# Performance work log

Hardware: AMD Instinct MI355X
Metric: run time of the kernel (lower is better)

## Reference

```python
import jax, jax.numpy as jnp
import numpy as np

N = 4096      # num_nodes (tokens)
D = 1024      # in_features
GC1 = 1024    # gc hidden sizes
GC2 = 1024
FC1 = 512     # fc hidden
NUM_CLASSES = 2
FW = 8        # forward band width
BW = 8        # backward band width


def setup_inputs() -> dict:
    key = jax.random.key(0)
    ks = jax.random.split(key, 6)
    s = 0.02
    return {
        "x": jax.random.normal(ks[0], (N, D), jnp.float32),
        # sequential band weights, initialized to 0.5 as in the module
        "fw_w": 0.5 * jnp.ones((FW,), jnp.float32),
        "bw_w": 0.5 * jnp.ones((BW,), jnp.float32),
        # graph-conv layer weights (linear: h @ W + b, then A @ .)
        "gc_w1": s * jax.random.normal(ks[1], (D, GC1), jnp.float32),
        "gc_b1": jnp.zeros((GC1,), jnp.float32),
        "gc_w2": s * jax.random.normal(ks[2], (GC1, GC2), jnp.float32),
        "gc_b2": jnp.zeros((GC2,), jnp.float32),
        # fully-connected head
        "fc_w1": s * jax.random.normal(ks[3], (GC2, FC1), jnp.float32),
        "fc_b1": jnp.zeros((FC1,), jnp.float32),
        "fc_w2": s * jax.random.normal(ks[4], (FC1, NUM_CLASSES), jnp.float32),
        "fc_b2": jnp.zeros((NUM_CLASSES,), jnp.float32),
    }


def build_adjacency(fw_w, bw_w, n):
    # banded adjacency: self-loops + forward superdiagonals + backward subdiagonals,
    # then symmetric normalization D^{-1/2} A D^{-1/2}
    a = jnp.eye(n, dtype=fw_w.dtype)
    for j in range(fw_w.shape[0]):          # small fixed band loop (FW)
        a = a + fw_w[j] * jnp.eye(n, k=j + 1, dtype=fw_w.dtype)
    for j in range(bw_w.shape[0]):          # small fixed band loop (BW)
        a = a + bw_w[j] * jnp.eye(n, k=-(j + 1), dtype=bw_w.dtype)
    d = a.sum(axis=1) ** -0.5               # row degrees
    return d[:, None] * a * d[None, :]


def reference(x, fw_w, bw_w, gc_w1, gc_b1, gc_w2, gc_b2, fc_w1, fc_b1, fc_w2, fc_b2):
    a = build_adjacency(fw_w, bw_w, x.shape[0])          # [N, N]
    # GC layers: selu(A @ (H W + b)); dropout=0.0 -> identity
    h = jax.nn.selu(a @ (x @ gc_w1 + gc_b1))             # [N, GC1]
    h = jax.nn.selu(a @ (h @ gc_w2 + gc_b2))             # [N, GC2]
    pooled = h.mean(axis=0)                              # mean pooling over nodes
    z = jax.nn.selu(pooled @ fc_w1 + fc_b1)              # [FC1]
    return z @ fc_w2 + fc_b2                             # [NUM_CLASSES] logits
```

## Files before the change

kernel.cpp:

```cpp
#include <hip/hip_runtime.h>
#include <stdint.h>

#define NND 4096
#define DIM 1024
#define FC1N 512

typedef __attribute__((ext_vector_type(8))) short short8;
typedef __attribute__((ext_vector_type(4))) float floatx4;
typedef unsigned short u16;
typedef unsigned int u32;

__device__ __forceinline__ u16 f2bf(float f) {
    union { float f; u32 u; } a; a.f = f;
    u32 u = a.u;
    return (u16)((u + 0x7fffu + ((u >> 16) & 1u)) >> 16);
}
__device__ __forceinline__ float bf2f(u16 h) {
    union { u32 u; float f; } a; a.u = ((u32)h) << 16; return a.f;
}
__device__ __forceinline__ float selu_f(float x) {
    const float lam = 1.0507009873554805f;
    const float alp = 1.6732632423543772f;
    return x > 0.f ? lam * x : lam * alp * (expf(x) - 1.f);
}
__device__ __forceinline__ void async16(const u16* g, u16* l) {
    __builtin_amdgcn_global_load_lds((const __attribute__((address_space(1))) u32*)g,
                                     (__attribute__((address_space(3))) u32*)l, 16, 0, 0);
}

__global__ void k_prep(const float* __restrict__ x, const float* __restrict__ w1,
                       const float* __restrict__ w2, u16* __restrict__ Xb,
                       u16* __restrict__ W1t, u16* __restrict__ W2t,
                       float* __restrict__ zero_base) {
    int b = blockIdx.x, t = threadIdx.x;
    if (b < 512) {
        const float4* xin = (const float4*)x;
        ushort4* xo = (ushort4*)Xb;
        int base = b * 2048 + t;
        #pragma unroll
        for (int i = 0; i < 8; ++i) {
            float4 v = xin[base + i * 256];
            ushort4 o; o.x = f2bf(v.x); o.y = f2bf(v.y); o.z = f2bf(v.z); o.w = f2bf(v.w);
            xo[base + i * 256] = o;
        }
        if (b == 0)
            for (int i = t; i < 1537; i += 256) zero_base[i] = 0.f;
        return;
    }
    int job = b - 512;
    const float* in = (job & 256) ? w2 : w1;
    u16* out = (job & 256) ? W2t : W1t;
    int tl = job & 255;
    int r0 = (tl >> 4) * 64, c0 = (tl & 15) * 64;
    __shared__ float tile[64][65];
    int cg = t & 15, rb = t >> 4;
    #pragma unroll
    for (int rr = 0; rr < 4; ++rr) {
        int row = rb + rr * 16;
        float4 v = *(const float4*)(in + (size_t)(r0 + row) * DIM + c0 + cg * 4);
        tile[row][cg * 4 + 0] = v.x; tile[row][cg * 4 + 1] = v.y;
        tile[row][cg * 4 + 2] = v.z; tile[row][cg * 4 + 3] = v.w;
    }
    __syncthreads();
    #pragma unroll
    for (int rr = 0; rr < 4; ++rr) {
        int nl = rb + rr * 16;
        int kl = cg * 4;
        ushort4 o;
        o.x = f2bf(tile[kl + 0][nl]); o.y = f2bf(tile[kl + 1][nl]);
        o.z = f2bf(tile[kl + 2][nl]); o.w = f2bf(tile[kl + 3][nl]);
        *(ushort4*)(out + (size_t)(c0 + nl) * DIM + r0 + kl) = o;
    }
}

__launch_bounds__(256, 4)
__global__ void k_gemmband(const u16* __restrict__ A, const u16* __restrict__ Bt,
                           const float* __restrict__ bias,
                           const float* __restrict__ fw, const float* __restrict__ bw,
                           u16* __restrict__ H, float* __restrict__ pooled, int mode) {
    __shared__ __align__(16) u16 stage[10240];
    __shared__ float sdinv_s[96];
    __shared__ float wt_s[17];
    __shared__ float pl[4][64];

    const int m0 = blockIdx.x * 64, n0 = blockIdx.y * 64;
    const int t = threadIdx.x, wave = t >> 6, lane = t & 63;
    const int q = lane >> 4, r = lane & 15;
    const int wm = wave & 1, wn = wave >> 1;
    const int Lrow = lane >> 3, Lseg = lane & 7;

    if (t < 96) {
        int g = m0 - 16 + t;
        float s = 0.f;
        if (g >= 0 && g < NND) {
            float deg = 1.f;
            #pragma unroll
            for (int j = 0; j < 8; ++j) {
                if (g + j + 1 < NND) deg += fw[j];
                if (g - j - 1 >= 0)  deg += bw[j];
            }
            s = 1.f / sqrtf(deg);
        }
        sdinv_s[t] = s;
    } else if (t >= 128 && t < 145) {
        int o = t - 136;
        wt_s[t - 128] = (o == 0) ? 1.f : (o > 0 ? fw[o - 1] : bw[-o - 1]);
    }

    floatx4 acc[3][2];
    #pragma unroll
    for (int mt = 0; mt < 3; ++mt) { acc[mt][0] = (floatx4)0.f; acc[mt][1] = (floatx4)0.f; }

    #pragma unroll 1
    for (int k = 0; k < 16; ++k) {
        int kb = k * 64;
        #pragma unroll
        for (int i = 0; i < 5; ++i) {
            int c = wave * 5 + i;
            u16* dst = &stage[c * 512];
            const u16* src;
            if (c < 12) {
                int row = c * 8 + Lrow;
                int g = m0 - 16 + row;
                g = g < 0 ? 0 : (g > NND - 1 ? NND - 1 : g);
                src = A + (size_t)g * DIM + kb + ((Lseg ^ Lrow) * 8);
            } else {
                int row = (c - 12) * 8 + Lrow;
                src = Bt + (size_t)(n0 + row) * DIM + kb + ((Lseg ^ Lrow) * 8);
            }
            async16(src, dst);
        }
        __syncthreads();
        const u16* As = &stage[0];
        const u16* Bs = &stage[6144];
        #pragma unroll
        for (int s = 0; s < 2; ++s) {
            int j0 = s * 4 + q;
            short8 bfr[2];
            #pragma unroll
            for (int nt = 0; nt < 2; ++nt) {
                int nl = wn * 32 + nt * 16 + r;
                bfr[nt] = *(const short8*)&Bs[nl * 64 + ((j0 ^ (nl & 7)) * 8)];
            }
            #pragma unroll
            for (int mt = 0; mt < 3; ++mt) {
                int ml = wm * 48 + mt * 16 + r;
                short8 afr = *(const short8*)&As[ml * 64 + ((j0 ^ (ml & 7)) * 8)];
                acc[mt][0] = __builtin_amdgcn_mfma_f32_16x16x32_bf16(afr, bfr[0], acc[mt][0], 0, 0, 0);
                acc[mt][1] = __builtin_amdgcn_mfma_f32_16x16x32_bf16(afr, bfr[1], acc[mt][1], 0, 0, 0);
            }
        }
        __syncthreads();
    }
    u16 (*Yt)[66] = (u16(*)[66])&stage[0];
    #pragma unroll
    for (int nt = 0; nt < 2; ++nt) {
        int col = wn * 32 + nt * 16 + r;
        float bv = bias[n0 + col];
        #pragma unroll
        for (int mt = 0; mt < 3; ++mt)
            #pragma unroll
            for (int rr = 0; rr < 4; ++rr)
                Yt[wm * 48 + mt * 16 + q * 4 + rr][col] = f2bf(acc[mt][nt][rr] + bv);
    }
    __syncthreads();

    int col = t & 63;
    int r0w = (t >> 6) * 16;
    float w[17];
    #pragma unroll
    for (int o = 0; o < 17; ++o) w[o] = wt_s[o];
    float win[17];
    #pragma unroll
    for (int j = 0; j < 16; ++j) {
        int T = r0w + 8 + j;
        win[j] = sdinv_s[T] * bf2f(Yt[T][col]);
    }
    float psum = 0.f;
    #pragma unroll
    for (int rr = 0; rr < 16; ++rr) {
        int T = r0w + 24 + rr;
        win[(rr + 16) % 17] = sdinv_s[T] * bf2f(Yt[T][col]);
        float a = 0.f;
        #pragma unroll
        for (int o = 0; o < 17; ++o) a += w[o] * win[(rr + o) % 17];
        float v = selu_f(a * sdinv_s[r0w + 16 + rr]);
        if (mode == 0) H[(size_t)(m0 + r0w + rr) * DIM + n0 + col] = f2bf(v);
        else psum += v;
    }
    if (mode) {
        pl[wave][col] = psum;
        __syncthreads();
        if (t < 64)
            atomicAdd(&pooled[n0 + t], pl[0][t] + pl[1][t] + pl[2][t] + pl[3][t]);
    }
}

__global__ void k_fc(const float* __restrict__ pooled, const float* __restrict__ fcw1,
                     const float* __restrict__ fcb1, const float* __restrict__ fcw2,
                     const float* __restrict__ fcb2, float* __restrict__ zacc,
                     u32* __restrict__ cnt, float* __restrict__ out) {
    __shared__ float red[1024];
    __shared__ int lastf;
    int o = threadIdx.x, b = blockIdx.x;
    int kb = b * 64;
    float s = 0.f;
    #pragma unroll 4
    for (int kk = 0; kk < 64; ++kk)
        s += pooled[kb + kk] * fcw1[(size_t)(kb + kk) * FC1N + o];
    atomicAdd(&zacc[o], s * (1.f / NND));
    __threadfence();
    __syncthreads();
    if (o == 0) lastf = (atomicAdd(cnt, 1u) == 15u);
    __syncthreads();
    if (!lastf) return;
    __threadfence();
    float zv = atomicAdd(&zacc[o], 0.f);
    float z = selu_f(zv + fcb1[o]);
    red[o] = z * fcw2[o * 2 + 0];
    red[512 + o] = z * fcw2[o * 2 + 1];
    __syncthreads();
    #pragma unroll 1
    for (int s2 = 256; s2 > 0; s2 >>= 1) {
        if (o < s2) { red[o] += red[o + s2]; red[512 + o] += red[512 + o + s2]; }
        __syncthreads();
    }
    if (o == 0) { out[0] = red[0] + fcb2[0]; out[1] = red[1] + fcb2[1]; }
}

extern "C" void kernel_launch(void* const* d_in, const int* in_sizes, int n_in,
                              void* d_out, int out_size, void* d_ws, size_t ws_size,
                              hipStream_t stream) {
    const float* x     = (const float*)d_in[0];
    const float* fw    = (const float*)d_in[1];
    const float* bw    = (const float*)d_in[2];
    const float* gc_w1 = (const float*)d_in[3];
    const float* gc_b1 = (const float*)d_in[4];
    const float* gc_w2 = (const float*)d_in[5];
    const float* gc_b2 = (const float*)d_in[6];
    const float* fc_w1 = (const float*)d_in[7];
    const float* fc_b1 = (const float*)d_in[8];
    const float* fc_w2 = (const float*)d_in[9];
    const float* fc_b2 = (const float*)d_in[10];
    float* out = (float*)d_out;

    char* ws = (char*)d_ws;
    u16*   Xb     = (u16*)(ws);
    u16*   H1     = (u16*)(ws + (8u  << 20));
    u16*   W1t    = (u16*)(ws + (16u << 20));
    u16*   W2t    = (u16*)(ws + (18u << 20));
    float* pooled = (float*)(ws + (20u << 20));
    float* zacc   = pooled + 1024;
    u32*   cnt    = (u32*)(zacc + 512);

    k_prep<<<1024, 256, 0, stream>>>(x, gc_w1, gc_w2, Xb, W1t, W2t, pooled);
    k_gemmband<<<dim3(64, 16), 256, 0, stream>>>(Xb, W1t, gc_b1, fw, bw, H1, nullptr, 0);
    k_gemmband<<<dim3(64, 16), 256, 0, stream>>>(H1, W2t, gc_b2, fw, bw, nullptr, pooled, 1);
    k_fc<<<16, 512, 0, stream>>>(pooled, fc_w1, fc_b1, fc_w2, fc_b2, zacc, cnt, out);
}
```

Baseline: 143.8 us.

## Load MFMA operands directly from global, halve block size, fuse FC head into GEMM

The GEMM kernel drops LDS staging with async global-to-LDS loads and barriers per K step. Instead, each of two waves reads bf16 A and B fragments straight from global memory into registers and runs a 48x64 MFMA tile. Blocks shrink to 128 threads, each computing 32 band rows. The separate FC kernel is folded into the second GEMM launch: the last 16 blocks to finish spin-wait on a counter, then compute the FC1 partial products, and the final block does the FC2 reduction. This removes LDS traffic, barriers and one launch, at the cost of uncoalesced or redundant global reads, since B fragments are reread per block without sharing, and of a spin-wait that relies on every block being resident or finishing.

```diff
diff --git a/kernel.cpp b/kernel.cpp
--- a/kernel.cpp
+++ b/kernel.cpp
@@ -22,10 +22,6 @@
     const float lam = 1.0507009873554805f;
     const float alp = 1.6732632423543772f;
     return x > 0.f ? lam * x : lam * alp * (expf(x) - 1.f);
-}
-__device__ __forceinline__ void async16(const u16* g, u16* l) {
-    __builtin_amdgcn_global_load_lds((const __attribute__((address_space(1))) u32*)g,
-                                     (__attribute__((address_space(3))) u32*)l, 16, 0, 0);
 }
 
 __global__ void k_prep(const float* __restrict__ x, const float* __restrict__ w1,
@@ -44,7 +40,7 @@
             xo[base + i * 256] = o;
         }
         if (b == 0)
-            for (int i = t; i < 1537; i += 256) zero_base[i] = 0.f;
+            for (int i = t; i < 1544; i += 256) zero_base[i] = 0.f;
         return;
     }
     int job = b - 512;
@@ -73,21 +69,24 @@
     }
 }
 
-__launch_bounds__(256, 4)
+__launch_bounds__(128, 4)
 __global__ void k_gemmband(const u16* __restrict__ A, const u16* __restrict__ Bt,
                            const float* __restrict__ bias,
                            const float* __restrict__ fw, const float* __restrict__ bw,
-                           u16* __restrict__ H, float* __restrict__ pooled, int mode) {
-    __shared__ __align__(16) u16 stage[10240];
+                           u16* __restrict__ H, float* __restrict__ pooled,
+                           const float* __restrict__ fcw1, const float* __restrict__ fcb1,
+                           const float* __restrict__ fcw2, const float* __restrict__ fcb2,
+                           float* __restrict__ zacc, u32* __restrict__ cnt,
+                           float* __restrict__ out, int mode) {
+    __shared__ __align__(16) u16 Yt[96][66];
     __shared__ float sdinv_s[96];
     __shared__ float wt_s[17];
-    __shared__ float pl[4][64];
+    __shared__ float pl[2][64];
+    __shared__ u32 ticket_s;
 
     const int m0 = blockIdx.x * 64, n0 = blockIdx.y * 64;
     const int t = threadIdx.x, wave = t >> 6, lane = t & 63;
     const int q = lane >> 4, r = lane & 15;
-    const int wm = wave & 1, wn = wave >> 1;
-    const int Lrow = lane >> 3, Lseg = lane & 7;
 
     if (t < 96) {
         int g = m0 - 16 + t;
@@ -102,71 +101,57 @@
             s = 1.f / sqrtf(deg);
         }
         sdinv_s[t] = s;
-    } else if (t >= 128 && t < 145) {
-        int o = t - 136;
-        wt_s[t - 128] = (o == 0) ? 1.f : (o > 0 ? fw[o - 1] : bw[-o - 1]);
-    }
-
-    floatx4 acc[3][2];
-    #pragma unroll
-    for (int mt = 0; mt < 3; ++mt) { acc[mt][0] = (floatx4)0.f; acc[mt][1] = (floatx4)0.f; }
-
-    #pragma unroll 1
-    for (int k = 0; k < 16; ++k) {
-        int kb = k * 64;
-        #pragma unroll
-        for (int i = 0; i < 5; ++i) {
-            int c = wave * 5 + i;
-            u16* dst = &stage[c * 512];
-            const u16* src;
-            if (c < 12) {
-                int row = c * 8 + Lrow;
-                int g = m0 - 16 + row;
-                g = g < 0 ? 0 : (g > NND - 1 ? NND - 1 : g);
-                src = A + (size_t)g * DIM + kb + ((Lseg ^ Lrow) * 8);
-            } else {
-                int row = (c - 12) * 8 + Lrow;
-                src = Bt + (size_t)(n0 + row) * DIM + kb + ((Lseg ^ Lrow) * 8);
-            }
-            async16(src, dst);
-        }
-        __syncthreads();
-        const u16* As = &stage[0];
-        const u16* Bs = &stage[6144];
-        #pragma unroll
-        for (int s = 0; s < 2; ++s) {
-            int j0 = s * 4 + q;
-            short8 bfr[2];
+    } else if (t < 113) {
+        int o = t - 104;
+        wt_s[t - 96] = (o == 0) ? 1.f : (o > 0 ? fw[o - 1] : bw[-o - 1]);
+    }
+
+    const u16* aptr[3];
+    #pragma unroll
+    for (int mt = 0; mt < 3; ++mt) {
+        int g = m0 - 16 + wave * 48 + mt * 16 + r;
+        g = g < 0 ? 0 : (g > NND - 1 ? NND - 1 : g);
+        aptr[mt] = A + (size_t)g * DIM + q * 8;
+    }
+    const u16* bptr[4];
+    #pragma unroll
+    for (int nt = 0; nt < 4; ++nt)
+        bptr[nt] = Bt + (size_t)(n0 + nt * 16 + r) * DIM + q * 8;
+
+    floatx4 acc[3][4];
+    #pragma unroll
+    for (int mt = 0; mt < 3; ++mt)
+        #pragma unroll
+        for (int nt = 0; nt < 4; ++nt) acc[mt][nt] = (floatx4)0.f;
+
+    #pragma unroll 4
+    for (int k0 = 0; k0 < DIM; k0 += 32) {
+        short8 bfr[4], afr[3];
+        #pragma unroll
+        for (int nt = 0; nt < 4; ++nt) bfr[nt] = *(const short8*)(bptr[nt] + k0);
+        #pragma unroll
+        for (int mt = 0; mt < 3; ++mt) afr[mt] = *(const short8*)(aptr[mt] + k0);
+        #pragma unroll
+        for (int mt = 0; mt < 3; ++mt)
             #pragma unroll
-            for (int nt = 0; nt < 2; ++nt) {
-                int nl = wn * 32 + nt * 16 + r;
-                bfr[nt] = *(const short8*)&Bs[nl * 64 + ((j0 ^ (nl & 7)) * 8)];
-            }
-            #pragma unroll
-            for (int mt = 0; mt < 3; ++mt) {
-                int ml = wm * 48 + mt * 16 + r;
-                short8 afr = *(const short8*)&As[ml * 64 + ((j0 ^ (ml & 7)) * 8)];
-                acc[mt][0] = __builtin_amdgcn_mfma_f32_16x16x32_bf16(afr, bfr[0], acc[mt][0], 0, 0, 0);
-                acc[mt][1] = __builtin_amdgcn_mfma_f32_16x16x32_bf16(afr, bfr[1], acc[mt][1], 0, 0, 0);
-            }
-        }
-        __syncthreads();
-    }
-    u16 (*Yt)[66] = (u16(*)[66])&stage[0];
-    #pragma unroll
-    for (int nt = 0; nt < 2; ++nt) {
-        int col = wn * 32 + nt * 16 + r;
+            for (int nt = 0; nt < 4; ++nt)
+                acc[mt][nt] = __builtin_amdgcn_mfma_f32_16x16x32_bf16(afr[mt], bfr[nt], acc[mt][nt], 0, 0, 0);
+    }
+
+    #pragma unroll
+    for (int nt = 0; nt < 4; ++nt) {
+        int col = nt * 16 + r;
         float bv = bias[n0 + col];
         #pragma unroll
         for (int mt = 0; mt < 3; ++mt)
             #pragma unroll
             for (int rr = 0; rr < 4; ++rr)
-                Yt[wm * 48 + mt * 16 + q * 4 + rr][col] = f2bf(acc[mt][nt][rr] + bv);
+                Yt[wave * 48 + mt * 16 + q * 4 + rr][col] = f2bf(acc[mt][nt][rr] + bv);
     }
     __syncthreads();
 
     int col = t & 63;
-    int r0w = (t >> 6) * 16;
+    int r0w = wave * 32;
     float w[17];
     #pragma unroll
     for (int o = 0; o < 17; ++o) w[o] = wt_s[o];
@@ -178,7 +163,7 @@
     }
     float psum = 0.f;
     #pragma unroll
-    for (int rr = 0; rr < 16; ++rr) {
+    for (int rr = 0; rr < 32; ++rr) {
         int T = r0w + 24 + rr;
         win[(rr + 16) % 17] = sdinv_s[T] * bf2f(Yt[T][col]);
         float a = 0.f;
@@ -188,44 +173,62 @@
         if (mode == 0) H[(size_t)(m0 + r0w + rr) * DIM + n0 + col] = f2bf(v);
         else psum += v;
     }
-    if (mode) {
-        pl[wave][col] = psum;
+    if (mode == 0) return;
+
+    pl[wave][col] = psum;
+    __syncthreads();
+    if (t < 64) atomicAdd(&pooled[n0 + t], pl[0][t] + pl[1][t]);
+    __threadfence();
+    __syncthreads();
+    if (t == 0) ticket_s = atomicAdd(&cnt[0], 1u);
+    __syncthreads();
+    u32 ticket = ticket_s;
+    if (ticket < 1024 - 16) return;
+    if (t == 0) {
+        while (__hip_atomic_load(&cnt[0], __ATOMIC_ACQUIRE, __HIP_MEMORY_SCOPE_AGENT) < 1024u)
+            __builtin_amdgcn_s_sleep(2);
+    }
+    __syncthreads();
+    __threadfence();
+    int kb = (int)(ticket - (1024 - 16)) * 64;
+    if (t < 64)
+        pl[0][t] = __hip_atomic_load(&pooled[kb + t], __ATOMIC_RELAXED,
+                                     __HIP_MEMORY_SCOPE_AGENT) * (1.f / NND);
+    __syncthreads();
+    float a0 = 0.f, a1 = 0.f, a2 = 0.f, a3 = 0.f;
+    #pragma unroll 8
+    for (int kk = 0; kk < 64; ++kk) {
+        float pv = pl[0][kk];
+        const float* wrow = fcw1 + (size_t)(kb + kk) * FC1N + t;
+        a0 += pv * wrow[0];   a1 += pv * wrow[128];
+        a2 += pv * wrow[256]; a3 += pv * wrow[384];
+    }
+    atomicAdd(&zacc[t], a0);       atomicAdd(&zacc[t + 128], a1);
+    atomicAdd(&zacc[t + 256], a2); atomicAdd(&zacc[t + 384], a3);
+    __threadfence();
+    __syncthreads();
+    if (t == 0) ticket_s = atomicAdd(&cnt[1], 1u);
+    __syncthreads();
+    if (ticket_s != 15) return;
+    __threadfence();
+    float r0p = 0.f, r1p = 0.f;
+    #pragma unroll
+    for (int i = 0; i < 4; ++i) {
+        int o = t + i * 128;
+        float zv = __hip_atomic_load(&zacc[o], __ATOMIC_RELAXED, __HIP_MEMORY_SCOPE_AGENT);
+        float z = selu_f(zv + fcb1[o]);
+        r0p += z * fcw2[o * 2 + 0];
+        r1p += z * fcw2[o * 2 + 1];
+    }
+    float* red = (float*)&Yt[0][0];
+    red[t] = r0p; red[128 + t] = r1p;
+    __syncthreads();
+    #pragma unroll 1
+    for (int s2 = 64; s2 > 0; s2 >>= 1) {
+        if (t < s2) { red[t] += red[t + s2]; red[128 + t] += red[128 + t + s2]; }
         __syncthreads();
-        if (t < 64)
-            atomicAdd(&pooled[n0 + t], pl[0][t] + pl[1][t] + pl[2][t] + pl[3][t]);
-    }
-}
-
-__global__ void k_fc(const float* __restrict__ pooled, const float* __restrict__ fcw1,
-                     const float* __restrict__ fcb1, const float* __restrict__ fcw2,
-                     const float* __restrict__ fcb2, float* __restrict__ zacc,
-                     u32* __restrict__ cnt, float* __restrict__ out) {
-    __shared__ float red[1024];
-    __shared__ int lastf;
-    int o = threadIdx.x, b = blockIdx.x;
-    int kb = b * 64;
-    float s = 0.f;
-    #pragma unroll 4
-    for (int kk = 0; kk < 64; ++kk)
-        s += pooled[kb + kk] * fcw1[(size_t)(kb + kk) * FC1N + o];
-    atomicAdd(&zacc[o], s * (1.f / NND));
-    __threadfence();
-    __syncthreads();
-    if (o == 0) lastf = (atomicAdd(cnt, 1u) == 15u);
-    __syncthreads();
-    if (!lastf) return;
-    __threadfence();
-    float zv = atomicAdd(&zacc[o], 0.f);
-    float z = selu_f(zv + fcb1[o]);
-    red[o] = z * fcw2[o * 2 + 0];
-    red[512 + o] = z * fcw2[o * 2 + 1];
-    __syncthreads();
-    #pragma unroll 1
-    for (int s2 = 256; s2 > 0; s2 >>= 1) {
-        if (o < s2) { red[o] += red[o + s2]; red[512 + o] += red[512 + o + s2]; }
-        __syncthreads();
-    }
-    if (o == 0) { out[0] = red[0] + fcb2[0]; out[1] = red[1] + fcb2[1]; }
+    }
+    if (t == 0) { out[0] = red[0] + fcb2[0]; out[1] = red[1] + fcb2[1]; }
 }
 
 extern "C" void kernel_launch(void* const* d_in, const int* in_sizes, int n_in,
@@ -254,7 +257,10 @@
     u32*   cnt    = (u32*)(zacc + 512);
 
     k_prep<<<1024, 256, 0, stream>>>(x, gc_w1, gc_w2, Xb, W1t, W2t, pooled);
-    k_gemmband<<<dim3(64, 16), 256, 0, stream>>>(Xb, W1t, gc_b1, fw, bw, H1, nullptr, 0);
-    k_gemmband<<<dim3(64, 16), 256, 0, stream>>>(H1, W2t, gc_b2, fw, bw, nullptr, pooled, 1);
-    k_fc<<<16, 512, 0, stream>>>(pooled, fc_w1, fc_b1, fc_w2, fc_b2, zacc, cnt, out);
-}
+    k_gemmband<<<dim3(64, 16), 128, 0, stream>>>(Xb, W1t, gc_b1, fw, bw, H1, nullptr,
+                                                 nullptr, nullptr, nullptr, nullptr,
+                                                 nullptr, nullptr, nullptr, 0);
+    k_gemmband<<<dim3(64, 16), 128, 0, stream>>>(H1, W2t, gc_b2, fw, bw, nullptr, pooled,
+                                                 fc_w1, fc_b1, fc_w2, fc_b2,
+                                                 zacc, cnt, out, 1);
+}
```

After: 254.9 us. 1.77x slower.

## Fuse FC head into second GC kernel via ticketed last-block reduction

Applied to the files above, without the earlier changes.

Drops the separate k_fc launch. The second GC kernel now writes per-block pooled partials instead of using atomicAdd. The last 16 blocks to finish, chosen by an atomic ticket, spin until every block has arrived, then each reduces one 64-column slice and applies fc_w1. A final ticketed block sums the 16 slices and computes the SELU and output logits. This removes one kernel launch and the pooled atomics, at the cost of a spin-wait and some serial tail work in a few blocks, and it relies on all 1024 blocks progressing forward while those blocks wait.

```diff
diff --git a/kernel.cpp b/kernel.cpp
--- a/kernel.cpp
+++ b/kernel.cpp
@@ -27,11 +27,17 @@
     __builtin_amdgcn_global_load_lds((const __attribute__((address_space(1))) u32*)g,
                                      (__attribute__((address_space(3))) u32*)l, 16, 0, 0);
 }
+__device__ __forceinline__ float gload(const float* p) {
+    return __hip_atomic_load(p, __ATOMIC_RELAXED, __HIP_MEMORY_SCOPE_AGENT);
+}
+__device__ __forceinline__ void gstore(float* p, float v) {
+    __hip_atomic_store(p, v, __ATOMIC_RELAXED, __HIP_MEMORY_SCOPE_AGENT);
+}
 
 __global__ void k_prep(const float* __restrict__ x, const float* __restrict__ w1,
                        const float* __restrict__ w2, u16* __restrict__ Xb,
                        u16* __restrict__ W1t, u16* __restrict__ W2t,
-                       float* __restrict__ zero_base) {
+                       u32* __restrict__ cnt) {
     int b = blockIdx.x, t = threadIdx.x;
     if (b < 512) {
         const float4* xin = (const float4*)x;
@@ -43,8 +49,7 @@
             ushort4 o; o.x = f2bf(v.x); o.y = f2bf(v.y); o.z = f2bf(v.z); o.w = f2bf(v.w);
             xo[base + i * 256] = o;
         }
-        if (b == 0)
-            for (int i = t; i < 1537; i += 256) zero_base[i] = 0.f;
+        if (b == 0 && t < 8) cnt[t] = 0u;
         return;
     }
     int job = b - 512;
@@ -77,11 +82,16 @@
 __global__ void k_gemmband(const u16* __restrict__ A, const u16* __restrict__ Bt,
                            const float* __restrict__ bias,
                            const float* __restrict__ fw, const float* __restrict__ bw,
-                           u16* __restrict__ H, float* __restrict__ pooled, int mode) {
+                           u16* __restrict__ H, float* __restrict__ Ppart,
+                           const float* __restrict__ fcw1, const float* __restrict__ fcb1,
+                           const float* __restrict__ fcw2, const float* __restrict__ fcb2,
+                           float* __restrict__ zpart, u32* __restrict__ cnt,
+                           float* __restrict__ out, int mode) {
     __shared__ __align__(16) u16 stage[10240];
     __shared__ float sdinv_s[96];
     __shared__ float wt_s[17];
     __shared__ float pl[4][64];
+    __shared__ u32 ticket_s;
 
     const int m0 = blockIdx.x * 64, n0 = blockIdx.y * 64;
     const int t = threadIdx.x, wave = t >> 6, lane = t & 63;
@@ -188,44 +198,72 @@
         if (mode == 0) H[(size_t)(m0 + r0w + rr) * DIM + n0 + col] = f2bf(v);
         else psum += v;
     }
-    if (mode) {
-        pl[wave][col] = psum;
+    if (mode == 0) return;
+
+    pl[wave][col] = psum;
+    __syncthreads();
+    if (t < 64)
+        gstore(&Ppart[(size_t)blockIdx.x * DIM + n0 + t],
+               ((pl[0][t] + pl[1][t]) + pl[2][t]) + pl[3][t]);
+    __threadfence();
+    __syncthreads();
+    if (t == 0) ticket_s = atomicAdd(&cnt[0], 1u);
+    __syncthreads();
+    u32 ticket = ticket_s;
+    if (ticket < 1024 - 16) return;
+    if (t == 0) {
+        while (__hip_atomic_load(&cnt[0], __ATOMIC_ACQUIRE, __HIP_MEMORY_SCOPE_AGENT) < 1024u)
+            __builtin_amdgcn_s_sleep(2);
+    }
+    __syncthreads();
+    __threadfence();
+    int slice = (int)(ticket - (1024 - 16));
+    int kb = slice * 64;
+    if (t < 64) {
+        float s = 0.f;
+        #pragma unroll 4
+        for (int bx = 0; bx < 64; ++bx)
+            s += gload(&Ppart[(size_t)bx * DIM + kb + t]);
+        pl[0][t] = s * (1.f / NND);
+    }
+    __syncthreads();
+    float a0 = 0.f, a1 = 0.f;
+    #pragma unroll 8
+    for (int kk = 0; kk < 64; ++kk) {
+        float pv = pl[0][kk];
+        const float* wrow = fcw1 + (size_t)(kb + kk) * FC1N + t;
+        a0 += pv * wrow[0];
+        a1 += pv * wrow[256];
+    }
+    gstore(&zpart[(size_t)slice * FC1N + t], a0);
+    gstore(&zpart[(size_t)slice * FC1N + t + 256], a1);
+    __threadfence();
+    __syncthreads();
+    if (t == 0) ticket_s = atomicAdd(&cnt[1], 1u);
+    __syncthreads();
+    if (ticket_s != 15) return;
+    __threadfence();
+    float r0p = 0.f, r1p = 0.f;
+    #pragma unroll
+    for (int i = 0; i < 2; ++i) {
+        int o = t + i * 256;
+        float zsum = 0.f;
+        #pragma unroll
+        for (int sidx = 0; sidx < 16; ++sidx)
+            zsum += gload(&zpart[(size_t)sidx * FC1N + o]);
+        float z = selu_f(zsum + fcb1[o]);
+        r0p += z * fcw2[o * 2 + 0];
+        r1p += z * fcw2[o * 2 + 1];
+    }
+    float* red = (float*)&stage[0];
+    red[t] = r0p; red[256 + t] = r1p;
+    __syncthreads();
+    #pragma unroll 1
+    for (int s2 = 128; s2 > 0; s2 >>= 1) {
+        if (t < s2) { red[t] += red[t + s2]; red[256 + t] += red[256 + t + s2]; }
         __syncthreads();
-        if (t < 64)
-            atomicAdd(&pooled[n0 + t], pl[0][t] + pl[1][t] + pl[2][t] + pl[3][t]);
-    }
-}
-
-__global__ void k_fc(const float* __restrict__ pooled, const float* __restrict__ fcw1,
-                     const float* __restrict__ fcb1, const float* __restrict__ fcw2,
-                     const float* __restrict__ fcb2, float* __restrict__ zacc,
-                     u32* __restrict__ cnt, float* __restrict__ out) {
-    __shared__ float red[1024];
-    __shared__ int lastf;
-    int o = threadIdx.x, b = blockIdx.x;
-    int kb = b * 64;
-    float s = 0.f;
-    #pragma unroll 4
-    for (int kk = 0; kk < 64; ++kk)
-        s += pooled[kb + kk] * fcw1[(size_t)(kb + kk) * FC1N + o];
-    atomicAdd(&zacc[o], s * (1.f / NND));
-    __threadfence();
-    __syncthreads();
-    if (o == 0) lastf = (atomicAdd(cnt, 1u) == 15u);
-    __syncthreads();
-    if (!lastf) return;
-    __threadfence();
-    float zv = atomicAdd(&zacc[o], 0.f);
-    float z = selu_f(zv + fcb1[o]);
-    red[o] = z * fcw2[o * 2 + 0];
-    red[512 + o] = z * fcw2[o * 2 + 1];
-    __syncthreads();
-    #pragma unroll 1
-    for (int s2 = 256; s2 > 0; s2 >>= 1) {
-        if (o < s2) { red[o] += red[o + s2]; red[512 + o] += red[512 + o + s2]; }
-        __syncthreads();
-    }
-    if (o == 0) { out[0] = red[0] + fcb2[0]; out[1] = red[1] + fcb2[1]; }
+    }
+    if (t == 0) { out[0] = red[0] + fcb2[0]; out[1] = red[1] + fcb2[1]; }
 }
 
 extern "C" void kernel_launch(void* const* d_in, const int* in_sizes, int n_in,
@@ -245,16 +283,19 @@
     float* out = (float*)d_out;
 
     char* ws = (char*)d_ws;
-    u16*   Xb     = (u16*)(ws);
-    u16*   H1     = (u16*)(ws + (8u  << 20));
-    u16*   W1t    = (u16*)(ws + (16u << 20));
-    u16*   W2t    = (u16*)(ws + (18u << 20));
-    float* pooled = (float*)(ws + (20u << 20));
-    float* zacc   = pooled + 1024;
-    u32*   cnt    = (u32*)(zacc + 512);
-
-    k_prep<<<1024, 256, 0, stream>>>(x, gc_w1, gc_w2, Xb, W1t, W2t, pooled);
-    k_gemmband<<<dim3(64, 16), 256, 0, stream>>>(Xb, W1t, gc_b1, fw, bw, H1, nullptr, 0);
-    k_gemmband<<<dim3(64, 16), 256, 0, stream>>>(H1, W2t, gc_b2, fw, bw, nullptr, pooled, 1);
-    k_fc<<<16, 512, 0, stream>>>(pooled, fc_w1, fc_b1, fc_w2, fc_b2, zacc, cnt, out);
-}
+    u16*   Xb    = (u16*)(ws);
+    u16*   H1    = (u16*)(ws + (8u  << 20));
+    u16*   W1t   = (u16*)(ws + (16u << 20));
+    u16*   W2t   = (u16*)(ws + (18u << 20));
+    float* Ppart = (float*)(ws + (20u << 20));
+    float* zpart = (float*)(ws + (20u << 20) + 262144);
+    u32*   cnt   = (u32*)(ws + (20u << 20) + 262144 + 32768);
+
+    k_prep<<<1024, 256, 0, stream>>>(x, gc_w1, gc_w2, Xb, W1t, W2t, cnt);
+    k_gemmband<<<dim3(64, 16), 256, 0, stream>>>(Xb, W1t, gc_b1, fw, bw, H1, nullptr,
+                                                 nullptr, nullptr, nullptr, nullptr,
+                                                 nullptr, nullptr, nullptr, 0);
+    k_gemmband<<<dim3(64, 16), 256, 0, stream>>>(H1, W2t, gc_b2, fw, bw, nullptr, Ppart,
+                                                 fc_w1, fc_b1, fc_w2, fc_b2,
+                                                 zpart, cnt, out, 1);
+}
```

Result: slower. 205.4 us (+42.8%).
